# Performance work log

Hardware: AMD Instinct MI355X
Metric: run time of the kernel (lower is better)

The kernel has to match this reference:

```python
import jax, jax.numpy as jnp
import numpy as np


def setup_inputs() -> dict:
    key = jax.random.key(0)
    ks = jax.random.split(key, 13)
    B, T, F = 4096, 512, 64
    P, M = 64, 64  # price / metrics embedding dims
    TD, ED = 1, 8  # target_dim, explanatory_dim
    s = 0.05
    return {
        "input_seq": jax.random.normal(ks[0], (B, T, F), jnp.float32),
        "m_Wih": jax.random.normal(ks[1], (M, F + P), jnp.float32) * s,
        "m_Whh": jax.random.normal(ks[2], (M, M), jnp.float32) * s,
        "m_bih": jax.random.normal(ks[3], (M,), jnp.float32) * s,
        "m_bhh": jax.random.normal(ks[4], (M,), jnp.float32) * s,
        "p_Wih": jax.random.normal(ks[5], (P, F + M), jnp.float32) * s,
        "p_Whh": jax.random.normal(ks[6], (P, P), jnp.float32) * s,
        "p_bih": jax.random.normal(ks[7], (P,), jnp.float32) * s,
        "p_bhh": jax.random.normal(ks[8], (P,), jnp.float32) * s,
        "price_lin_W": jax.random.normal(ks[9], (TD, P), jnp.float32) * s,
        "price_lin_b": jax.random.normal(ks[10], (TD,), jnp.float32) * s,
        "metrics_lin_W": jax.random.normal(ks[11], (ED, M), jnp.float32) * s,
        "metrics_lin_b": jax.random.normal(ks[12], (ED,), jnp.float32) * s,
    }


def reference(input_seq, m_Wih, m_Whh, m_bih, m_bhh,
              p_Wih, p_Whh, p_bih, p_bhh,
              price_lin_W, price_lin_b, metrics_lin_W, metrics_lin_b):
    B = input_seq.shape[0]
    P = p_Whh.shape[0]
    M = m_Whh.shape[0]
    p0 = jnp.zeros((B, P), input_seq.dtype)
    m0 = jnp.zeros((B, M), input_seq.dtype)

    def step(carry, x_t):  # x_t: [B, F]
        p, m = carry
        # metrics cell: input = cat(x_t, price_embedding)
        m = jnp.tanh(jnp.concatenate([x_t, p], axis=1) @ m_Wih.T + m_bih
                     + m @ m_Whh.T + m_bhh)
        # price cell: input = cat(x_t, metrics_embedding)
        p = jnp.tanh(jnp.concatenate([x_t, m], axis=1) @ p_Wih.T + p_bih
                     + p @ p_Whh.T + p_bhh)
        return (p, m), None

    (p, m), _ = jax.lax.scan(step, (p0, m0), jnp.swapaxes(input_seq, 0, 1))
    # dropout in eval mode = identity
    price_pred = p @ price_lin_W.T + price_lin_b
    metrics_pred = m @ metrics_lin_W.T + metrics_lin_b
    return (price_pred, metrics_pred)
```

## Files before the change

### kernel.cpp

```cpp
#include <hip/hip_runtime.h>

typedef short bf16x8 __attribute__((ext_vector_type(8)));
typedef float f32x4 __attribute__((ext_vector_type(4)));
typedef int   int4v  __attribute__((ext_vector_type(4)));

#define MFMA16(a, b, c) __builtin_amdgcn_mfma_f32_16x16x32_bf16((a), (b), (c), 0, 0, 0)

static constexpr int T_LEN = 512;
static constexpr int F_DIM = 64;
static constexpr int NB    = 8;
static constexpr float C1  = 2.885390081777927f;

__device__ __forceinline__ unsigned short brne(float f) {
  unsigned u = __float_as_uint(f);
  return (unsigned short)((u + 0x7fffu + ((u >> 16) & 1u)) >> 16);
}

__device__ __forceinline__ int cvtpk(float lo, float hi) {
  int r;
  asm("v_cvt_pk_bf16_f32 %0, %1, %2" : "=v"(r) : "v"(lo), "v"(hi));
  return r;
}

__device__ __forceinline__ bf16x8 cvt8(const float4 &a, const float4 &b) {
  int4v d = {cvtpk(a.x, a.y), cvtpk(a.z, a.w), cvtpk(b.x, b.y), cvtpk(b.z, b.w)};
  union { int4v i; bf16x8 h; } u;
  u.i = d;
  return u.h;
}

__device__ __forceinline__ void swap32(float &a, float &b) {
  auto r = __builtin_amdgcn_permlane32_swap(__float_as_int(a), __float_as_int(b),
                                            false, false);
  a = __int_as_float(r[0]);
  b = __int_as_float(r[1]);
}

__device__ __forceinline__ float xor1(float v) {
  return __int_as_float(__builtin_amdgcn_mov_dpp(__float_as_int(v), 0xB1, 0xF, 0xF, true));
}

__device__ __forceinline__ float tanh_fold(float s, float c2) {
  float e  = __builtin_amdgcn_exp2f(__builtin_fmaf(s, C1, c2));
  float rc = __builtin_amdgcn_rcpf(e + 1.0f);
  return __builtin_fmaf(-2.0f, rc, 1.0f);
}

template<int PAR, bool FIN>
__device__ __forceinline__ void epilogue(
    const f32x4 &a0, const f32x4 &a1, float c2,
    unsigned short (*buf)[72], float (*fin)[68],
    int wofs, bool evn, int rowA, int j)
{
  float z0 = a0[0] + a1[0];
  float z1 = a0[1] + a1[1];
  float z2 = a0[2] + a1[2];
  float z3 = a0[3] + a1[3];
  swap32(z0, z2);
  swap32(z1, z3);
  float sA = (PAR == 0) ? z0 : z2;
  float sB = (PAR == 0) ? z1 : z3;
  float tA = tanh_fold(sA, c2);
  float tB = tanh_fold(sB, c2);
  float nA = xor1(tA);
  float nB = xor1(tB);
  if (evn) {
    unsigned short *p = &buf[0][0];
    *(unsigned *)(p + wofs)      = (unsigned)cvtpk(tA, nA);
    *(unsigned *)(p + wofs + 72) = (unsigned)cvtpk(tB, nB);
  }
  if (FIN) {
    fin[rowA][j]     = tA;
    fin[rowA + 1][j] = tB;
  }
}

template<int PAR, bool FIN>
__device__ __forceinline__ void step_cells(
    int arow, int g8, int j, int wofs, bool evn, int rowA,
    const bf16x8 &x0, const bf16x8 &x1,
    bf16x8 &mo0, bf16x8 &mo1,
    const bf16x8 (&Bm)[6], const bf16x8 (&Bp)[6],
    float c2m, float c2p, const f32x4 &Z,
    unsigned short (*sm)[72],
    unsigned short (*sp_c)[72], unsigned short (*sp_p)[72],
    float (*mfin)[68], float (*pfin)[68])
{
  bf16x8 p0 = *(const bf16x8 *)&sp_p[arow][g8];
  bf16x8 p1 = *(const bf16x8 *)&sp_p[arow][32 + g8];

  __builtin_amdgcn_s_setprio(1);
  {
    f32x4 a0 = MFMA16(x0, Bm[0], Z);
    f32x4 a1 = MFMA16(x1, Bm[1], Z);
    a0 = MFMA16(p0, Bm[2], a0);
    a1 = MFMA16(p1, Bm[3], a1);
    a0 = MFMA16(mo0, Bm[4], a0);
    a1 = MFMA16(mo1, Bm[5], a1);
    epilogue<PAR, FIN>(a0, a1, c2m, sm, mfin, wofs, evn, rowA, j);
  }
  __builtin_amdgcn_s_setprio(0);
  __syncthreads();
  {
    bf16x8 n0 = *(const bf16x8 *)&sm[arow][g8];
    bf16x8 n1 = *(const bf16x8 *)&sm[arow][32 + g8];
    __builtin_amdgcn_s_setprio(1);
    f32x4 b0 = MFMA16(x0, Bp[0], Z);
    f32x4 b1 = MFMA16(x1, Bp[1], Z);
    b0 = MFMA16(n0, Bp[2], b0);
    b1 = MFMA16(n1, Bp[3], b1);
    b0 = MFMA16(p0, Bp[4], b0);
    b1 = MFMA16(p1, Bp[5], b1);
    epilogue<PAR, FIN>(b0, b1, c2p, sp_c, pfin, wofs, evn, rowA, j);
    __builtin_amdgcn_s_setprio(0);
    mo0 = n0;
    mo1 = n1;
  }
  __syncthreads();
}

__global__ __launch_bounds__(256, 2)
void mr_rnn_kernel(const float *__restrict__ x,
                   const float *__restrict__ mWih, const float *__restrict__ mWhh,
                   const float *__restrict__ mbih, const float *__restrict__ mbhh,
                   const float *__restrict__ pWih, const float *__restrict__ pWhh,
                   const float *__restrict__ pbih, const float *__restrict__ pbhh,
                   const float *__restrict__ plW,  const float *__restrict__ plb,
                   const float *__restrict__ mlW,  const float *__restrict__ mlb,
                   float *__restrict__ out, int B)
{
  __shared__ __align__(16) unsigned short sm[NB][72];
  __shared__ __align__(16) unsigned short sp[2][NB][72];
  __shared__ __align__(16) float s_mfin[NB][68], s_pfin[NB][68];

  const int tid  = threadIdx.x;
  const int lane = tid & 63;
  const int q    = tid >> 6;
  const int l15  = lane & 15;
  const int arow = l15 & (NB - 1);
  const int half = l15 >> 3;
  const int g    = lane >> 4;
  const int j    = q * 16 + l15;
  const int b0   = blockIdx.x * NB;
  const int g8   = g * 8;
  const int rowA = ((lane & 16) >> 2) | ((lane >> 5) << 1);
  const bool evn = (l15 & 1) == 0;
  const int wofs = rowA * 72 + (j & ~1);

  bf16x8 Bm[6], Bp[6];
#pragma unroll
  for (int kt = 0; kt < 6; ++kt) {
    const int k0 = kt * 32 + g8;
#pragma unroll
    for (int i = 0; i < 8; ++i) {
      const int k = k0 + i;
      float wm = (k < 128) ? mWih[j * 128 + k] : mWhh[j * 64 + (k - 128)];
      float wp = (k < 128) ? pWih[j * 128 + k] : pWhh[j * 64 + (k - 128)];
      Bm[kt][i] = (short)brne(wm);
      Bp[kt][i] = (short)brne(wp);
    }
  }
  const float c2m = C1 * (mbih[j] + mbhh[j]);
  const float c2p = C1 * (pbih[j] + pbhh[j]);
  const f32x4 Z = {0.f, 0.f, 0.f, 0.f};

  for (int idx = tid; idx < NB * 72; idx += 256) {
    const int bb = idx / 72, kk = idx % 72;
    sp[1][bb][kk] = 0;
  }
  bf16x8 mo0 = {0, 0, 0, 0, 0, 0, 0, 0};
  bf16x8 mo1 = {0, 0, 0, 0, 0, 0, 0, 0};

  const float *pxl = x + ((size_t)(b0 + arow) * T_LEN + half) * F_DIM + g8;
  float4 A0 = *(const float4 *)(pxl);
  float4 A1 = *(const float4 *)(pxl + 4);
  float4 A2 = *(const float4 *)(pxl + 32);
  float4 A3 = *(const float4 *)(pxl + 36);
  bf16x8 x0 = cvt8(A0, A1);
  bf16x8 x1 = cvt8(A2, A3);
  __syncthreads();

#pragma unroll 1
  for (int t = 0; t < T_LEN - 2; t += 2) {
    pxl += 2 * F_DIM;
    A0 = *(const float4 *)(pxl);
    A1 = *(const float4 *)(pxl + 4);
    A2 = *(const float4 *)(pxl + 32);
    A3 = *(const float4 *)(pxl + 36);
    step_cells<0, false>(arow, g8, j, wofs, evn, rowA, x0, x1, mo0, mo1,
                         Bm, Bp, c2m, c2p, Z,
                         sm, sp[0], sp[1], s_mfin, s_pfin);
    step_cells<1, false>(arow, g8, j, wofs, evn, rowA, x0, x1, mo0, mo1,
                         Bm, Bp, c2m, c2p, Z,
                         sm, sp[1], sp[0], s_mfin, s_pfin);
    x0 = cvt8(A0, A1);
    x1 = cvt8(A2, A3);
  }
  step_cells<0, false>(arow, g8, j, wofs, evn, rowA, x0, x1, mo0, mo1,
                       Bm, Bp, c2m, c2p, Z,
                       sm, sp[0], sp[1], s_mfin, s_pfin);
  step_cells<1, true>(arow, g8, j, wofs, evn, rowA, x0, x1, mo0, mo1,
                      Bm, Bp, c2m, c2p, Z,
                      sm, sp[1], sp[0], s_mfin, s_pfin);

  if (tid < NB) {
    const int b = tid;
    float acc = plb[0];
#pragma unroll 1
    for (int k = 0; k < 64; ++k) acc += s_pfin[b][k] * plW[k];
    out[b0 + b] = acc;
  } else if (tid < NB + NB * 8) {
    const int r = tid - NB;
    const int b = r >> 3, e = r & 7;
    float acc = mlb[e];
#pragma unroll 1
    for (int k = 0; k < 64; ++k) acc += s_mfin[b][k] * mlW[e * 64 + k];
    out[(size_t)B + (size_t)(b0 + b) * 8 + e] = acc;
  }
}

extern "C" void kernel_launch(void* const* d_in, const int* in_sizes, int n_in,
                              void* d_out, int out_size, void* d_ws, size_t ws_size,
                              hipStream_t stream) {
  (void)n_in; (void)out_size; (void)d_ws; (void)ws_size;
  const float* x    = (const float*)d_in[0];
  const float* mWih = (const float*)d_in[1];
  const float* mWhh = (const float*)d_in[2];
  const float* mbih = (const float*)d_in[3];
  const float* mbhh = (const float*)d_in[4];
  const float* pWih = (const float*)d_in[5];
  const float* pWhh = (const float*)d_in[6];
  const float* pbih = (const float*)d_in[7];
  const float* pbhh = (const float*)d_in[8];
  const float* plW  = (const float*)d_in[9];
  const float* plb  = (const float*)d_in[10];
  const float* mlW  = (const float*)d_in[11];
  const float* mlb  = (const float*)d_in[12];
  const int B = in_sizes[0] / (T_LEN * F_DIM);
  const int nblk = B / NB;
  mr_rnn_kernel<<<dim3(nblk), dim3(256), 0, stream>>>(
      x, mWih, mWhh, mbih, mbhh, pWih, pWhh, pbih, pbhh,
      plW, plb, mlW, mlb, (float*)d_out, B);
}
```

Before: 270.3 us.

## Process 16 batch rows per block to fill MFMA rows and simplify epilogue

Doubles the batch rows per block from 8 to 16, so every row of the 16x16 MFMA tile holds real data instead of processing two timesteps' worth of duplicate rows. This removes the permlane swap, DPP exchange and even-lane packed writes, and each lane now writes four scalar bf16 results per step using a cheaper round-half-up conversion. Barriers become a raw s_barrier with an explicit lgkmcnt wait, and x loads for the next steps are double-buffered one step further ahead. Blocks drop to half as many, with launch bounds allowing one block per SIMD group, which reduces occupancy and latency hiding, and the rounding mode changes slightly.

Result: faster. 263.9 us, median of 2 (-2.4%).

```diff
diff --git a/kernel.cpp b/kernel.cpp
--- a/kernel.cpp
+++ b/kernel.cpp
@@ -8,12 +8,16 @@
 
 static constexpr int T_LEN = 512;
 static constexpr int F_DIM = 64;
-static constexpr int NB    = 8;
+static constexpr int NB    = 16;
 static constexpr float C1  = 2.885390081777927f;
 
 __device__ __forceinline__ unsigned short brne(float f) {
   unsigned u = __float_as_uint(f);
   return (unsigned short)((u + 0x7fffu + ((u >> 16) & 1u)) >> 16);
+}
+
+__device__ __forceinline__ unsigned short rhu(float f) {
+  return (unsigned short)((__float_as_uint(f) + 0x8000u) >> 16);
 }
 
 __device__ __forceinline__ int cvtpk(float lo, float hi) {
@@ -29,55 +33,21 @@
   return u.h;
 }
 
-__device__ __forceinline__ void swap32(float &a, float &b) {
-  auto r = __builtin_amdgcn_permlane32_swap(__float_as_int(a), __float_as_int(b),
-                                            false, false);
-  a = __int_as_float(r[0]);
-  b = __int_as_float(r[1]);
-}
-
-__device__ __forceinline__ float xor1(float v) {
-  return __int_as_float(__builtin_amdgcn_mov_dpp(__float_as_int(v), 0xB1, 0xF, 0xF, true));
-}
-
 __device__ __forceinline__ float tanh_fold(float s, float c2) {
   float e  = __builtin_amdgcn_exp2f(__builtin_fmaf(s, C1, c2));
   float rc = __builtin_amdgcn_rcpf(e + 1.0f);
   return __builtin_fmaf(-2.0f, rc, 1.0f);
 }
 
-template<int PAR, bool FIN>
-__device__ __forceinline__ void epilogue(
-    const f32x4 &a0, const f32x4 &a1, float c2,
-    unsigned short (*buf)[72], float (*fin)[68],
-    int wofs, bool evn, int rowA, int j)
-{
-  float z0 = a0[0] + a1[0];
-  float z1 = a0[1] + a1[1];
-  float z2 = a0[2] + a1[2];
-  float z3 = a0[3] + a1[3];
-  swap32(z0, z2);
-  swap32(z1, z3);
-  float sA = (PAR == 0) ? z0 : z2;
-  float sB = (PAR == 0) ? z1 : z3;
-  float tA = tanh_fold(sA, c2);
-  float tB = tanh_fold(sB, c2);
-  float nA = xor1(tA);
-  float nB = xor1(tB);
-  if (evn) {
-    unsigned short *p = &buf[0][0];
-    *(unsigned *)(p + wofs)      = (unsigned)cvtpk(tA, nA);
-    *(unsigned *)(p + wofs + 72) = (unsigned)cvtpk(tB, nB);
-  }
-  if (FIN) {
-    fin[rowA][j]     = tA;
-    fin[rowA + 1][j] = tB;
-  }
-}
-
-template<int PAR, bool FIN>
+__device__ __forceinline__ void bar() {
+  asm volatile("s_waitcnt lgkmcnt(0)" ::: "memory");
+  __builtin_amdgcn_s_barrier();
+  __builtin_amdgcn_sched_barrier(0);
+}
+
+template<bool FIN>
 __device__ __forceinline__ void step_cells(
-    int arow, int g8, int j, int wofs, bool evn, int rowA,
+    int arow, int g8, int j, int rowb,
     const bf16x8 &x0, const bf16x8 &x1,
     bf16x8 &mo0, bf16x8 &mo1,
     const bf16x8 (&Bm)[6], const bf16x8 (&Bp)[6],
@@ -89,7 +59,6 @@
   bf16x8 p0 = *(const bf16x8 *)&sp_p[arow][g8];
   bf16x8 p1 = *(const bf16x8 *)&sp_p[arow][32 + g8];
 
-  __builtin_amdgcn_s_setprio(1);
   {
     f32x4 a0 = MFMA16(x0, Bm[0], Z);
     f32x4 a1 = MFMA16(x1, Bm[1], Z);
@@ -97,29 +66,36 @@
     a1 = MFMA16(p1, Bm[3], a1);
     a0 = MFMA16(mo0, Bm[4], a0);
     a1 = MFMA16(mo1, Bm[5], a1);
-    epilogue<PAR, FIN>(a0, a1, c2m, sm, mfin, wofs, evn, rowA, j);
-  }
-  __builtin_amdgcn_s_setprio(0);
-  __syncthreads();
+#pragma unroll
+    for (int r = 0; r < 4; ++r) {
+      float tv = tanh_fold(a0[r] + a1[r], c2m);
+      sm[rowb + r][j] = rhu(tv);
+      if (FIN) mfin[rowb + r][j] = tv;
+    }
+  }
+  bar();
   {
     bf16x8 n0 = *(const bf16x8 *)&sm[arow][g8];
     bf16x8 n1 = *(const bf16x8 *)&sm[arow][32 + g8];
-    __builtin_amdgcn_s_setprio(1);
     f32x4 b0 = MFMA16(x0, Bp[0], Z);
     f32x4 b1 = MFMA16(x1, Bp[1], Z);
     b0 = MFMA16(n0, Bp[2], b0);
     b1 = MFMA16(n1, Bp[3], b1);
     b0 = MFMA16(p0, Bp[4], b0);
     b1 = MFMA16(p1, Bp[5], b1);
-    epilogue<PAR, FIN>(b0, b1, c2p, sp_c, pfin, wofs, evn, rowA, j);
-    __builtin_amdgcn_s_setprio(0);
+#pragma unroll
+    for (int r = 0; r < 4; ++r) {
+      float tv = tanh_fold(b0[r] + b1[r], c2p);
+      sp_c[rowb + r][j] = rhu(tv);
+      if (FIN) pfin[rowb + r][j] = tv;
+    }
     mo0 = n0;
     mo1 = n1;
   }
-  __syncthreads();
-}
-
-__global__ __launch_bounds__(256, 2)
+  bar();
+}
+
+__global__ __launch_bounds__(256, 1)
 void mr_rnn_kernel(const float *__restrict__ x,
                    const float *__restrict__ mWih, const float *__restrict__ mWhh,
                    const float *__restrict__ mbih, const float *__restrict__ mbhh,
@@ -137,15 +113,12 @@
   const int lane = tid & 63;
   const int q    = tid >> 6;
   const int l15  = lane & 15;
-  const int arow = l15 & (NB - 1);
-  const int half = l15 >> 3;
+  const int arow = l15;
   const int g    = lane >> 4;
   const int j    = q * 16 + l15;
   const int b0   = blockIdx.x * NB;
   const int g8   = g * 8;
-  const int rowA = ((lane & 16) >> 2) | ((lane >> 5) << 1);
-  const bool evn = (l15 & 1) == 0;
-  const int wofs = rowA * 72 + (j & ~1);
+  const int rowb = g * 4;
 
   bf16x8 Bm[6], Bp[6];
 #pragma unroll
@@ -171,37 +144,50 @@
   bf16x8 mo0 = {0, 0, 0, 0, 0, 0, 0, 0};
   bf16x8 mo1 = {0, 0, 0, 0, 0, 0, 0, 0};
 
-  const float *pxl = x + ((size_t)(b0 + arow) * T_LEN + half) * F_DIM + g8;
-  float4 A0 = *(const float4 *)(pxl);
-  float4 A1 = *(const float4 *)(pxl + 4);
-  float4 A2 = *(const float4 *)(pxl + 32);
-  float4 A3 = *(const float4 *)(pxl + 36);
-  bf16x8 x0 = cvt8(A0, A1);
-  bf16x8 x1 = cvt8(A2, A3);
+  const float *pxl = x + (size_t)(b0 + arow) * T_LEN * F_DIM + g8;
+  float4 Q0 = *(const float4 *)(pxl);
+  float4 Q1 = *(const float4 *)(pxl + 4);
+  float4 Q2 = *(const float4 *)(pxl + 32);
+  float4 Q3 = *(const float4 *)(pxl + 36);
+  bf16x8 x0 = cvt8(Q0, Q1);
+  bf16x8 x1 = cvt8(Q2, Q3);
+  float4 R0 = *(const float4 *)(pxl + F_DIM);
+  float4 R1 = *(const float4 *)(pxl + F_DIM + 4);
+  float4 R2 = *(const float4 *)(pxl + F_DIM + 32);
+  float4 R3 = *(const float4 *)(pxl + F_DIM + 36);
   __syncthreads();
 
 #pragma unroll 1
   for (int t = 0; t < T_LEN - 2; t += 2) {
-    pxl += 2 * F_DIM;
-    A0 = *(const float4 *)(pxl);
-    A1 = *(const float4 *)(pxl + 4);
-    A2 = *(const float4 *)(pxl + 32);
-    A3 = *(const float4 *)(pxl + 36);
-    step_cells<0, false>(arow, g8, j, wofs, evn, rowA, x0, x1, mo0, mo1,
-                         Bm, Bp, c2m, c2p, Z,
-                         sm, sp[0], sp[1], s_mfin, s_pfin);
-    step_cells<1, false>(arow, g8, j, wofs, evn, rowA, x0, x1, mo0, mo1,
-                         Bm, Bp, c2m, c2p, Z,
-                         sm, sp[1], sp[0], s_mfin, s_pfin);
-    x0 = cvt8(A0, A1);
-    x1 = cvt8(A2, A3);
-  }
-  step_cells<0, false>(arow, g8, j, wofs, evn, rowA, x0, x1, mo0, mo1,
-                       Bm, Bp, c2m, c2p, Z,
-                       sm, sp[0], sp[1], s_mfin, s_pfin);
-  step_cells<1, true>(arow, g8, j, wofs, evn, rowA, x0, x1, mo0, mo1,
+    Q0 = *(const float4 *)(pxl + 2 * F_DIM);
+    Q1 = *(const float4 *)(pxl + 2 * F_DIM + 4);
+    Q2 = *(const float4 *)(pxl + 2 * F_DIM + 32);
+    Q3 = *(const float4 *)(pxl + 2 * F_DIM + 36);
+    step_cells<false>(arow, g8, j, rowb, x0, x1, mo0, mo1,
+                      Bm, Bp, c2m, c2p, Z,
+                      sm, sp[0], sp[1], s_mfin, s_pfin);
+    x0 = cvt8(R0, R1);
+    x1 = cvt8(R2, R3);
+    R0 = *(const float4 *)(pxl + 3 * F_DIM);
+    R1 = *(const float4 *)(pxl + 3 * F_DIM + 4);
+    R2 = *(const float4 *)(pxl + 3 * F_DIM + 32);
+    R3 = *(const float4 *)(pxl + 3 * F_DIM + 36);
+    step_cells<false>(arow, g8, j, rowb, x0, x1, mo0, mo1,
                       Bm, Bp, c2m, c2p, Z,
                       sm, sp[1], sp[0], s_mfin, s_pfin);
+    x0 = cvt8(Q0, Q1);
+    x1 = cvt8(Q2, Q3);
+    pxl += 2 * F_DIM;
+  }
+  step_cells<false>(arow, g8, j, rowb, x0, x1, mo0, mo1,
+                    Bm, Bp, c2m, c2p, Z,
+                    sm, sp[0], sp[1], s_mfin, s_pfin);
+  x0 = cvt8(R0, R1);
+  x1 = cvt8(R2, R3);
+  step_cells<true>(arow, g8, j, rowb, x0, x1, mo0, mo1,
+                   Bm, Bp, c2m, c2p, Z,
+                   sm, sp[1], sp[0], s_mfin, s_pfin);
+  __syncthreads();
 
   if (tid < NB) {
     const int b = tid;
```
